# Optimization experiments

Hardware: AMD Instinct MI355X
Metric: run time of the kernel (lower is better)

## Reference

```python
import jax, jax.numpy as jnp
import jax.lax as lax
import numpy as np

G = 128    # number of asset groups (batch)
A = 100    # n_assets per group
WIN = 10   # window_size
FD = 16    # feature_dim
H = 128    # hidden_dim


def setup_inputs() -> dict:
    key = jax.random.key(0)
    ks = jax.random.split(key, 12)
    N = G * A
    def glorot(k, shape, fan_in):
        return (jax.random.normal(k, shape, jnp.float32) / np.sqrt(fan_in)).astype(jnp.float32)
    return {
        "x": jax.random.normal(ks[0], (N, WIN, FD), jnp.float32),
        "W1": glorot(ks[1], (WIN * FD, H), WIN * FD),
        "b1": jnp.zeros((H,), jnp.float32),
        "W2": glorot(ks[2], (H, H), H),
        "b2": jnp.zeros((H,), jnp.float32),
        "W3": glorot(ks[3], (H, H), H),
        "b3": jnp.zeros((H,), jnp.float32),
        "cw1": glorot(ks[4], (H, 1, 1, 3), 3),      # conv2d_1 weight [out,in,kh,kw]
        "cb1": jnp.zeros((H,), jnp.float32),
        "cw2": glorot(ks[5], (1, H, 1, 3), 3 * H),  # conv2d_2 weight
        "cb2": jnp.zeros((1,), jnp.float32),
    }


def _corrcoef(r):
    xc = r - r.mean(axis=1, keepdims=True)
    cov = xc @ xc.T                      # divisor cancels in correlation
    d = jnp.sqrt(jnp.diag(cov))
    return cov / (d[:, None] * d[None, :])


def _conv1x3(h, w, b):
    # h: [1,C,N,H]; kernel (1,3), padding (0,1) -> NCHW conv
    out = lax.conv_general_dilated(h, w, (1, 1), ((0, 0), (1, 1)),
                                   dimension_numbers=("NCHW", "OIHW", "NCHW"))
    return out + b[None, :, None, None]


def reference(x, W1, b1, W2, b2, W3, b3, cw1, cb1, cw2, cb2):
    # block-diagonal adjacency == independent per-group adjacencies
    returns = x[:, :, -1].reshape(G, A, WIN)
    corr = jax.vmap(_corrcoef)(returns)                  # [G,A,A]
    adj = 1.0 - jnp.abs(corr) + jnp.eye(A, dtype=x.dtype)
    dinv = 1.0 / jnp.sqrt(adj.sum(axis=-1))              # [G,A]
    norm_adj = dinv[:, :, None] * adj * dinv[:, None, :] # D^-1/2 A D^-1/2

    feats = x.reshape(G, A, WIN * FD)
    h = jax.nn.relu(jnp.einsum("gij,gjf->gif", norm_adj, feats) @ W1 + b1)
    h = jax.nn.relu(jnp.einsum("gij,gjh->gih", norm_adj, h) @ W2 + b2)
    h = jax.nn.relu(jnp.einsum("gij,gjh->gih", norm_adj, h) @ W3 + b3)

    h = h.reshape(1, 1, G * A, H)                        # [1,1,N,H]
    h = jax.nn.relu(_conv1x3(h, cw1, cb1))               # [1,H,N,H]
    out = _conv1x3(h, cw2, cb2)                          # [1,1,N,H]
    return out[0, 0]                                     # [N,H]
```

## Files before the change

### kernel.cpp

```cpp
#include <hip/hip_runtime.h>

#define G   128
#define A   100
#define WIN 10
#define FD  16
#define H   128
#define NROWS (G*A)
#define K1  (WIN*FD)

#define SST 136
#define YST 136
#define AST 40
#define H3ST 132

typedef __attribute__((ext_vector_type(8))) short short8;
typedef __attribute__((ext_vector_type(4))) short short4v;
typedef __attribute__((ext_vector_type(4))) float floatx4;

struct BfPair { short h, l; };

__device__ inline unsigned short f2bf(float f) {
    unsigned u = __float_as_uint(f);
    u += 0x7fff + ((u >> 16) & 1);
    return (unsigned short)(u >> 16);
}
__device__ inline float bf2f(unsigned short h) {
    return __uint_as_float(((unsigned)h) << 16);
}
__device__ inline BfPair split1(float v) {
    BfPair p;
    unsigned short hb = f2bf(v);
    p.h = (short)hb;
    p.l = (short)f2bf(v - bf2f(hb));
    return p;
}

__global__ __launch_bounds__(1024) void k_mega(
    const float* __restrict__ x,
    const float* __restrict__ W1, const float* __restrict__ b1,
    const float* __restrict__ W2, const float* __restrict__ b2,
    const float* __restrict__ W3, const float* __restrict__ b3,
    const float* __restrict__ cw1, const float* __restrict__ cb1,
    const float* __restrict__ cw2, const float* __restrict__ cb2,
    float* __restrict__ out)
{
    __shared__ short Ybuf[2 * 128 * YST];
    __shared__ short Sbuf[2 * 112 * SST];
    __shared__ short Abuf[2 * 112 * AST];
    __shared__ float wbuf[H][8];
    __shared__ float xcT[WIN][104];
    __shared__ float invn[A];
    __shared__ float dinv[A];

    short* Yh = Ybuf;            short* Yl = Ybuf + 128 * YST;
    short* Sh = Sbuf;            short* Sl = Sbuf + 112 * SST;
    short* Ah = Abuf;            short* Al = Abuf + 112 * AST;
    float* adjs = (float*)Ybuf;
    float* h3f  = (float*)Sbuf;

    const int g = blockIdx.x >> 1, half = blockIdx.x & 1;
    const int t = threadIdx.x;
    const int wvid = t >> 6, lane = t & 63;
    const int quad = lane >> 4, r16 = lane & 15;

    if (t < H) {
        *(float4*)&wbuf[t][0] = make_float4(cw1[3*t], cw1[3*t+1], cw1[3*t+2], cb1[t]);
        *(float4*)&wbuf[t][4] = make_float4(cw2[3*t], cw2[3*t+1], cw2[3*t+2], cb2[0]);
    }
    for (int e = t; e < A * WIN; e += 1024) {
        int a = e / WIN, wv = e % WIN;
        xcT[wv][a] = x[((g * A + a) * WIN + wv) * FD + (FD - 1)];
    }
    __syncthreads();
    if (t < A) {
        float m = 0.f;
        #pragma unroll
        for (int wv = 0; wv < WIN; wv++) m += xcT[wv][t];
        m *= (1.0f / WIN);
        float ss = 0.f;
        #pragma unroll
        for (int wv = 0; wv < WIN; wv++) {
            float v = xcT[wv][t] - m;
            xcT[wv][t] = v;
            ss += v * v;
        }
        invn[t] = rsqrtf(ss);
    }
    __syncthreads();
    for (int e = t; e < 2500; e += 1024) {
        int ti = e / 50, tj = e % 50;
        int i0 = 2 * ti, j0v = 2 * tj;
        float d00 = 0.f, d01 = 0.f, d10 = 0.f, d11 = 0.f;
        #pragma unroll
        for (int wv = 0; wv < WIN; wv++) {
            float2 xi = *(const float2*)&xcT[wv][i0];
            float2 xj = *(const float2*)&xcT[wv][j0v];
            d00 = fmaf(xi.x, xj.x, d00); d01 = fmaf(xi.x, xj.y, d01);
            d10 = fmaf(xi.y, xj.x, d10); d11 = fmaf(xi.y, xj.y, d11);
        }
        float ii0 = invn[i0], ii1 = invn[i0 + 1];
        float ij0 = invn[j0v], ij1 = invn[j0v + 1];
        float e2 = (ti == tj) ? 1.f : 0.f;
        adjs[i0 * 101 + j0v]           = 1.f - fabsf(d00 * ii0 * ij0) + e2;
        adjs[i0 * 101 + j0v + 1]       = 1.f - fabsf(d01 * ii0 * ij1);
        adjs[(i0 + 1) * 101 + j0v]     = 1.f - fabsf(d10 * ii1 * ij0);
        adjs[(i0 + 1) * 101 + j0v + 1] = 1.f - fabsf(d11 * ii1 * ij1) + e2;
    }
    __syncthreads();
    if (t < A) {
        float s = 0.f;
        for (int j = 0; j < A; j++) s += adjs[t * 101 + j];
        dinv[t] = rsqrtf(s);
    }
    __syncthreads();
    for (int e = t; e < 112 * 64; e += 1024) {
        int m = e >> 6, k2 = (e & 63) * 2;
        float v0 = (m < A && k2 < A)     ? dinv[m] * adjs[m * 101 + k2]     * dinv[k2]     : 0.f;
        float v1 = (m < A && k2 + 1 < A) ? dinv[m] * adjs[m * 101 + k2 + 1] * dinv[k2 + 1] : 0.f;
        BfPair p0 = split1(v0), p1 = split1(v1);
        *(short2*)&Sh[m * SST + k2] = make_short2(p0.h, p1.h);
        *(short2*)&Sl[m * SST + k2] = make_short2(p0.l, p1.l);
    }
    if (t < 384) {
        int r = 100 + (t >> 5), c = t & 31;
        Ah[r * AST + c] = 0; Al[r * AST + c] = 0;
    }
    __syncthreads();
    for (int e = t; e < 2048; e += 1024) {
        int n = e >> 4, k = 112 + (e & 15);
        Yh[n * YST + k] = 0; Yl[n * YST + k] = 0;
    }

    const int ntA  = wvid & 7;
    const int mtlo = (wvid < 8) ? 0 : 4;
    const int mcnt = (wvid < 8) ? 4 : 3;
    const int mtB  = wvid >> 1;
    const int ntB0 = (wvid & 1) * 4;

    for (int layer = 0; layer < 3; layer++) {
        const float* Wg = (layer == 0) ? W1 : (layer == 1) ? W2 : W3;
        const float* bg = (layer == 0) ? b1 : (layer == 1) ? b2 : b3;
        const int nch = (layer == 0) ? 5 : 4;

        floatx4 acc[4];
        #pragma unroll
        for (int i = 0; i < 4; i++) acc[i] = (floatx4)0.f;

        for (int c = 0; c < nch; c++) {
            const int k0 = c << 5;
            short8 bh, bl;
            {
                const float* wp = Wg + (size_t)(k0 + quad * 8) * H + ntA * 16 + r16;
                #pragma unroll
                for (int i = 0; i < 8; i++) {
                    BfPair p = split1(wp[(size_t)i * H]);
                    bh[i] = p.h; bl[i] = p.l;
                }
            }
            if (layer == 0) {
                __syncthreads();
                if (t < 800) {
                    int r = t >> 3, q = t & 7;
                    float4 f = *(const float4*)(x + (size_t)(g * A + r) * K1 + k0 + q * 4);
                    float v[4] = {f.x, f.y, f.z, f.w};
                    short4v hh, ll;
                    #pragma unroll
                    for (int i = 0; i < 4; i++) {
                        BfPair p = split1(v[i]);
                        hh[i] = p.h; ll[i] = p.l;
                    }
                    *(short4v*)&Ah[r * AST + q * 4] = hh;
                    *(short4v*)&Al[r * AST + q * 4] = ll;
                }
                __syncthreads();
                for (int mi = 0; mi < mcnt; mi++) {
                    int mt = mtlo + mi;
                    short8 ah = *(const short8*)&Ah[(mt * 16 + r16) * AST + quad * 8];
                    short8 al = *(const short8*)&Al[(mt * 16 + r16) * AST + quad * 8];
                    acc[mi] = __builtin_amdgcn_mfma_f32_16x16x32_bf16(ah, bh, acc[mi], 0, 0, 0);
                    acc[mi] = __builtin_amdgcn_mfma_f32_16x16x32_bf16(ah, bl, acc[mi], 0, 0, 0);
                    acc[mi] = __builtin_amdgcn_mfma_f32_16x16x32_bf16(al, bh, acc[mi], 0, 0, 0);
                }
            } else {
                for (int mi = 0; mi < mcnt; mi++) {
                    int mt = mtlo + mi;
                    short8 ah = *(const short8*)&Yh[(mt * 16 + r16) * YST + k0 + quad * 8];
                    short8 al = *(const short8*)&Yl[(mt * 16 + r16) * YST + k0 + quad * 8];
                    acc[mi] = __builtin_amdgcn_mfma_f32_16x16x32_bf16(ah, bh, acc[mi], 0, 0, 0);
                    acc[mi] = __builtin_amdgcn_mfma_f32_16x16x32_bf16(ah, bl, acc[mi], 0, 0, 0);
                    acc[mi] = __builtin_amdgcn_mfma_f32_16x16x32_bf16(al, bh, acc[mi], 0, 0, 0);
                }
            }
        }
        __syncthreads();

        for (int mi = 0; mi < mcnt; mi++) {
            int mt = mtlo + mi;
            short4v yh4, yl4;
            #pragma unroll
            for (int rr = 0; rr < 4; rr++) {
                BfPair p = split1(acc[mi][rr]);
                yh4[rr] = p.h; yl4[rr] = p.l;
            }
            int off = (ntA * 16 + r16) * YST + mt * 16 + quad * 4;
            *(short4v*)&Yh[off] = yh4;
            *(short4v*)&Yl[off] = yl4;
        }
        __syncthreads();

        floatx4 accB[4];
        #pragma unroll
        for (int i = 0; i < 4; i++) accB[i] = (floatx4)0.f;
        if (mtB < 7) {
            #pragma unroll
            for (int c = 0; c < 4; c++) {
                const int k0 = c << 5;
                short8 ah = *(const short8*)&Sh[(mtB * 16 + r16) * SST + k0 + quad * 8];
                short8 al = *(const short8*)&Sl[(mtB * 16 + r16) * SST + k0 + quad * 8];
                #pragma unroll
                for (int j = 0; j < 4; j++) {
                    int nt = ntB0 + j;
                    short8 yh8 = *(const short8*)&Yh[(nt * 16 + r16) * YST + k0 + quad * 8];
                    short8 yl8 = *(const short8*)&Yl[(nt * 16 + r16) * YST + k0 + quad * 8];
                    accB[j] = __builtin_amdgcn_mfma_f32_16x16x32_bf16(ah, yh8, accB[j], 0, 0, 0);
                    accB[j] = __builtin_amdgcn_mfma_f32_16x16x32_bf16(ah, yl8, accB[j], 0, 0, 0);
                    accB[j] = __builtin_amdgcn_mfma_f32_16x16x32_bf16(al, yh8, accB[j], 0, 0, 0);
                }
            }
        }
        __syncthreads();

        if (mtB < 7) {
            #pragma unroll
            for (int j = 0; j < 4; j++) {
                int n = (ntB0 + j) * 16 + r16;
                float bv = bg[n];
                #pragma unroll
                for (int rr = 0; rr < 4; rr++) {
                    int m = mtB * 16 + quad * 4 + rr;
                    float v = fmaxf(0.f, accB[j][rr] + bv);
                    if (layer < 2) {
                        BfPair p = split1(v);
                        Yh[m * YST + n] = p.h;
                        Yl[m * YST + n] = p.l;
                    } else if (m < A) {
                        h3f[m * H3ST + n] = v;
                    }
                }
            }
        }
        __syncthreads();
    }

    const int slot = t >> 5, q = t & 31;
    const int j0 = q * 4;
    const float mlo = (q == 0)  ? 0.f : 1.f;
    const float mhi = (q == 31) ? 0.f : 1.f;
    const float c2b = wbuf[0][7];
    #pragma unroll
    for (int it = 0; it < 2; it++) {
        int rl = it * 32 + slot;
        if (rl < 50) {
            int r = half * 50 + rl;
            const float* hr = h3f + (size_t)r * H3ST;
            float hh[8];
            if (q == 0) {
                hh[0] = 0.f; hh[1] = 0.f;
                #pragma unroll
                for (int i = 0; i < 6; i++) hh[2 + i] = hr[i];
            } else if (q == 31) {
                #pragma unroll
                for (int i = 0; i < 6; i++) hh[i] = hr[122 + i];
                hh[6] = 0.f; hh[7] = 0.f;
            } else {
                #pragma unroll
                for (int i = 0; i < 8; i++) hh[i] = hr[j0 - 2 + i];
            }
            float acc4[4] = {0.f, 0.f, 0.f, 0.f};
            #pragma unroll 4
            for (int c = 0; c < H; c++) {
                float4 wA = *(const float4*)&wbuf[c][0];
                float4 wB = *(const float4*)&wbuf[c][4];
                float tt[6];
                #pragma unroll
                for (int m2 = 0; m2 < 6; m2++)
                    tt[m2] = fmaxf(0.f, fmaf(wA.z, hh[m2 + 2],
                                        fmaf(wA.y, hh[m2 + 1],
                                        fmaf(wA.x, hh[m2], wA.w))));
                tt[0] *= mlo; tt[5] *= mhi;
                #pragma unroll
                for (int p2 = 0; p2 < 4; p2++)
                    acc4[p2] = fmaf(wB.x, tt[p2],
                               fmaf(wB.y, tt[p2 + 1],
                               fmaf(wB.z, tt[p2 + 2], acc4[p2])));
            }
            *(float4*)(out + ((size_t)g * A + r) * H + j0) =
                make_float4(acc4[0] + c2b, acc4[1] + c2b, acc4[2] + c2b, acc4[3] + c2b);
        }
    }
}

extern "C" void kernel_launch(void* const* d_in, const int* in_sizes, int n_in,
                              void* d_out, int out_size, void* d_ws, size_t ws_size,
                              hipStream_t stream) {
    const float* x   = (const float*)d_in[0];
    const float* W1  = (const float*)d_in[1];
    const float* b1  = (const float*)d_in[2];
    const float* W2  = (const float*)d_in[3];
    const float* b2  = (const float*)d_in[4];
    const float* W3  = (const float*)d_in[5];
    const float* b3  = (const float*)d_in[6];
    const float* cw1 = (const float*)d_in[7];
    const float* cb1 = (const float*)d_in[8];
    const float* cw2 = (const float*)d_in[9];
    const float* cb2 = (const float*)d_in[10];
    float* out = (float*)d_out;

    k_mega<<<G * 2, 1024, 0, stream>>>(x, W1, b1, W2, b2, W3, b3,
                                       cw1, cb1, cw2, cb2, out);
}
```

Baseline: 166.8 us.

## Pre-split weights into transposed bf16 hi/lo and vectorize conv epilogue with packed FMA

Adds a small prep kernel that converts W1..W3 once into transposed bf16 hi/lo arrays in workspace, so each of the 256 mega blocks loads ready-made short8 fragments instead of doing strided fp32 loads and splits. The conv epilogue is restructured so each thread produces 8 outputs over channel pairs using packed 2-wide float FMAs, with conv weights re-laid out as interleaved pairs. This cuts redundant weight conversion and raises arithmetic density in the conv stage, at the cost of an extra kernel launch.

```diff
diff --git a/kernel.cpp b/kernel.cpp
--- a/kernel.cpp
+++ b/kernel.cpp
@@ -16,6 +16,7 @@
 typedef __attribute__((ext_vector_type(8))) short short8;
 typedef __attribute__((ext_vector_type(4))) short short4v;
 typedef __attribute__((ext_vector_type(4))) float floatx4;
+typedef __attribute__((ext_vector_type(2))) float pf2;
 
 struct BfPair { short h, l; };
 
@@ -35,11 +36,32 @@
     return p;
 }
 
+__global__ __launch_bounds__(256) void k_prep(const float* __restrict__ W1,
+                                              const float* __restrict__ W2,
+                                              const float* __restrict__ W3,
+                                              short* __restrict__ Wh,
+                                              short* __restrict__ Wl) {
+    const int b = blockIdx.x, t = threadIdx.x;
+    int l, kc;
+    const float* Wsrc;
+    if (b < 10)      { l = 0; kc = b;      Wsrc = W1; }
+    else if (b < 18) { l = 1; kc = b - 10; Wsrc = W2; }
+    else             { l = 2; kc = b - 18; Wsrc = W3; }
+    short* dh = Wh + l * 128 * 160;
+    short* dl = Wl + l * 128 * 160;
+    for (int e = t; e < 16 * 128; e += 256) {
+        int k = kc * 16 + (e >> 7), n = e & 127;
+        BfPair p = split1(Wsrc[(size_t)k * H + n]);
+        dh[n * 160 + k] = p.h;
+        dl[n * 160 + k] = p.l;
+    }
+}
+
 __global__ __launch_bounds__(1024) void k_mega(
     const float* __restrict__ x,
-    const float* __restrict__ W1, const float* __restrict__ b1,
-    const float* __restrict__ W2, const float* __restrict__ b2,
-    const float* __restrict__ W3, const float* __restrict__ b3,
+    const short* __restrict__ Whg, const short* __restrict__ Wlg,
+    const float* __restrict__ b1, const float* __restrict__ b2,
+    const float* __restrict__ b3,
     const float* __restrict__ cw1, const float* __restrict__ cb1,
     const float* __restrict__ cw2, const float* __restrict__ cb2,
     float* __restrict__ out)
@@ -47,7 +69,7 @@
     __shared__ short Ybuf[2 * 128 * YST];
     __shared__ short Sbuf[2 * 112 * SST];
     __shared__ short Abuf[2 * 112 * AST];
-    __shared__ float wbuf[H][8];
+    __shared__ float wp2[64][16];
     __shared__ float xcT[WIN][104];
     __shared__ float invn[A];
     __shared__ float dinv[A];
@@ -64,8 +86,15 @@
     const int quad = lane >> 4, r16 = lane & 15;
 
     if (t < H) {
-        *(float4*)&wbuf[t][0] = make_float4(cw1[3*t], cw1[3*t+1], cw1[3*t+2], cb1[t]);
-        *(float4*)&wbuf[t][4] = make_float4(cw2[3*t], cw2[3*t+1], cw2[3*t+2], cb2[0]);
+        int cp = t >> 1, par = t & 1;
+        wp2[cp][0  + par] = cw1[3 * t];
+        wp2[cp][2  + par] = cw1[3 * t + 1];
+        wp2[cp][4  + par] = cw1[3 * t + 2];
+        wp2[cp][6  + par] = cb1[t];
+        wp2[cp][8  + par] = cw2[3 * t];
+        wp2[cp][10 + par] = cw2[3 * t + 1];
+        wp2[cp][12 + par] = cw2[3 * t + 2];
+        wp2[cp][14 + par] = cb2[0];
     }
     for (int e = t; e < A * WIN; e += 1024) {
         int a = e / WIN, wv = e % WIN;
@@ -138,8 +167,9 @@
     const int ntB0 = (wvid & 1) * 4;
 
     for (int layer = 0; layer < 3; layer++) {
-        const float* Wg = (layer == 0) ? W1 : (layer == 1) ? W2 : W3;
         const float* bg = (layer == 0) ? b1 : (layer == 1) ? b2 : b3;
+        const short* wh = Whg + layer * 128 * 160;
+        const short* wl = Wlg + layer * 128 * 160;
         const int nch = (layer == 0) ? 5 : 4;
 
         floatx4 acc[4];
@@ -148,15 +178,9 @@
 
         for (int c = 0; c < nch; c++) {
             const int k0 = c << 5;
-            short8 bh, bl;
-            {
-                const float* wp = Wg + (size_t)(k0 + quad * 8) * H + ntA * 16 + r16;
-                #pragma unroll
-                for (int i = 0; i < 8; i++) {
-                    BfPair p = split1(wp[(size_t)i * H]);
-                    bh[i] = p.h; bl[i] = p.l;
-                }
-            }
+            size_t wo = (size_t)(ntA * 16 + r16) * 160 + k0 + quad * 8;
+            short8 bh = *(const short8*)(wh + wo);
+            short8 bl = *(const short8*)(wl + wo);
             if (layer == 0) {
                 __syncthreads();
                 if (t < 800) {
@@ -252,51 +276,65 @@
         __syncthreads();
     }
 
-    const int slot = t >> 5, q = t & 31;
-    const int j0 = q * 4;
-    const float mlo = (q == 0)  ? 0.f : 1.f;
-    const float mhi = (q == 31) ? 0.f : 1.f;
-    const float c2b = wbuf[0][7];
-    #pragma unroll
-    for (int it = 0; it < 2; it++) {
-        int rl = it * 32 + slot;
-        if (rl < 50) {
-            int r = half * 50 + rl;
-            const float* hr = h3f + (size_t)r * H3ST;
-            float hh[8];
-            if (q == 0) {
-                hh[0] = 0.f; hh[1] = 0.f;
-                #pragma unroll
-                for (int i = 0; i < 6; i++) hh[2 + i] = hr[i];
-            } else if (q == 31) {
-                #pragma unroll
-                for (int i = 0; i < 6; i++) hh[i] = hr[122 + i];
-                hh[6] = 0.f; hh[7] = 0.f;
-            } else {
-                #pragma unroll
-                for (int i = 0; i < 8; i++) hh[i] = hr[j0 - 2 + i];
-            }
-            float acc4[4] = {0.f, 0.f, 0.f, 0.f};
-            #pragma unroll 4
-            for (int c = 0; c < H; c++) {
-                float4 wA = *(const float4*)&wbuf[c][0];
-                float4 wB = *(const float4*)&wbuf[c][4];
-                float tt[6];
-                #pragma unroll
-                for (int m2 = 0; m2 < 6; m2++)
-                    tt[m2] = fmaxf(0.f, fmaf(wA.z, hh[m2 + 2],
-                                        fmaf(wA.y, hh[m2 + 1],
-                                        fmaf(wA.x, hh[m2], wA.w))));
-                tt[0] *= mlo; tt[5] *= mhi;
-                #pragma unroll
-                for (int p2 = 0; p2 < 4; p2++)
-                    acc4[p2] = fmaf(wB.x, tt[p2],
-                               fmaf(wB.y, tt[p2 + 1],
-                               fmaf(wB.z, tt[p2 + 2], acc4[p2])));
-            }
-            *(float4*)(out + ((size_t)g * A + r) * H + j0) =
-                make_float4(acc4[0] + c2b, acc4[1] + c2b, acc4[2] + c2b, acc4[3] + c2b);
-        }
+    if (t < 800) {
+        const int row = t >> 4, q = t & 15;
+        const int j0 = q * 8;
+        const int r = half * 50 + row;
+        const float* hr = h3f + (size_t)r * H3ST;
+
+        float hh[12];
+        if (q == 0) {
+            hh[0] = 0.f; hh[1] = 0.f;
+            #pragma unroll
+            for (int i = 0; i < 10; i++) hh[2 + i] = hr[i];
+        } else if (q == 15) {
+            #pragma unroll
+            for (int i = 0; i < 10; i++) hh[i] = hr[118 + i];
+            hh[10] = 0.f; hh[11] = 0.f;
+        } else {
+            #pragma unroll
+            for (int i = 0; i < 12; i++) hh[i] = hr[j0 - 2 + i];
+        }
+        const pf2 mlo2 = (pf2)((q == 0)  ? 0.f : 1.f);
+        const pf2 mhi2 = (pf2)((q == 15) ? 0.f : 1.f);
+        const pf2 zero2 = (pf2)0.f;
+
+        pf2 accp[8];
+        #pragma unroll
+        for (int p = 0; p < 8; p++) accp[p] = zero2;
+
+        #pragma unroll 2
+        for (int cp = 0; cp < 64; cp++) {
+            pf2 w0 = *(const pf2*)&wp2[cp][0];
+            pf2 w1 = *(const pf2*)&wp2[cp][2];
+            pf2 w2 = *(const pf2*)&wp2[cp][4];
+            pf2 bb = *(const pf2*)&wp2[cp][6];
+            pf2 v0 = *(const pf2*)&wp2[cp][8];
+            pf2 v1 = *(const pf2*)&wp2[cp][10];
+            pf2 v2 = *(const pf2*)&wp2[cp][12];
+            pf2 tt[10];
+            #pragma unroll
+            for (int m = 0; m < 10; m++) {
+                pf2 s = __builtin_elementwise_fma(w2, (pf2)hh[m + 2],
+                        __builtin_elementwise_fma(w1, (pf2)hh[m + 1],
+                        __builtin_elementwise_fma(w0, (pf2)hh[m], bb)));
+                tt[m] = __builtin_elementwise_max(s, zero2);
+            }
+            tt[0] *= mlo2;
+            tt[9] *= mhi2;
+            #pragma unroll
+            for (int p = 0; p < 8; p++)
+                accp[p] = __builtin_elementwise_fma(v0, tt[p],
+                          __builtin_elementwise_fma(v1, tt[p + 1],
+                          __builtin_elementwise_fma(v2, tt[p + 2], accp[p])));
+        }
+        const float c2b = wp2[0][14];
+        float o[8];
+        #pragma unroll
+        for (int p = 0; p < 8; p++) o[p] = accp[p].x + accp[p].y + c2b;
+        float* op = out + ((size_t)g * A + r) * H + j0;
+        *(float4*)op       = make_float4(o[0], o[1], o[2], o[3]);
+        *(float4*)(op + 4) = make_float4(o[4], o[5], o[6], o[7]);
     }
 }
 
@@ -316,6 +354,10 @@
     const float* cb2 = (const float*)d_in[10];
     float* out = (float*)d_out;
 
-    k_mega<<<G * 2, 1024, 0, stream>>>(x, W1, b1, W2, b2, W3, b3,
+    short* Wh = (short*)d_ws;
+    short* Wl = Wh + 3 * 128 * 160;
+
+    k_prep<<<26, 256, 0, stream>>>(W1, W2, W3, Wh, Wl);
+    k_mega<<<G * 2, 1024, 0, stream>>>(x, Wh, Wl, b1, b2, b3,
                                        cw1, cb1, cw2, cb2, out);
 }
```

Measured after the change: 162.5 us. -2.6%, faster.
